# Performance work log

Hardware: AMD Instinct MI355X
Metric: run time of the kernel (lower is better)

Reference implementation:

```python
import jax, jax.numpy as jnp
import numpy as np
import math

NN_K = 32          # num_neighbor = ceil(k/dilation) = 32
MAP_SIZE = 32
GROUP = 4


def _fibonacci_sphere(samples):
    # matches fibonacci_sphere(samples, randomize=False): rnd = 1.0
    pts = [[0.0, 0.0, 0.0]]
    offset = 2.0 / samples
    increment = math.pi * (3.0 - math.sqrt(5.0))
    for i in range(samples - 1):
        y = i * offset - 1 + offset / 2.0
        r = math.sqrt(1.0 - y * y)
        phi = ((i + 1.0) % samples) * increment
        pts.append([math.cos(phi) * r, y, math.sin(phi) * r])
    return np.asarray(pts, dtype=np.float32)


def setup_inputs() -> dict:
    B, N, C_in, C_out = 8, 2048, 64, 128
    key = jax.random.key(0)
    ks = jax.random.split(key, 6)
    x = jax.random.normal(ks[0], (B, 3, N), dtype=jnp.float32)
    feature = jax.random.normal(ks[1], (B, C_in, N), dtype=jnp.float32)
    neigh_indexs = jax.random.randint(ks[2], (B, N, NN_K), 0, N, dtype=jnp.int32)
    B_rff = jax.random.normal(ks[3], (7, MAP_SIZE), dtype=jnp.float32)  # frozen RFF proj
    kernels = jnp.asarray(_fibonacci_sphere(NN_K).T)                    # [3, NN_K], frozen
    mlp_w = jax.random.normal(ks[4], (C_in, 2 * MAP_SIZE), dtype=jnp.float32) * 0.05
    mlp_b = jnp.zeros((C_in,), dtype=jnp.float32)
    conv_w = jax.random.normal(ks[5], (C_out, 2 * C_in * NN_K), dtype=jnp.float32) * 0.02
    conv_b = jnp.zeros((C_out,), dtype=jnp.float32)
    return {"x": x, "feature": feature, "neigh_indexs": neigh_indexs,
            "B_rff": B_rff, "kernels": kernels,
            "mlp_w": mlp_w, "mlp_b": mlp_b, "conv_w": conv_w, "conv_b": conv_b}


def _topkmax(perm):
    # two normalization passes over axis=1 (rows), squaring in between, then hard threshold
    perm = perm / (jnp.sum(perm, axis=1, keepdims=True) + 1e-6)
    perm = perm * perm
    perm = perm / (jnp.sum(perm, axis=1, keepdims=True) + 1e-6)
    return jnp.where(perm > 0.1, perm, 0.0)


def _paiconv(x, feature, neigh_indexs, B_rff, kernels, mlp_w, mlp_b, conv_w, conv_b):
    bsz, C, N = feature.shape           # B, num_feat, num_pts
    nn_k = neigh_indexs.shape[-1]
    xp = jnp.transpose(x, (0, 2, 1))    # [B, N, 3]

    # neighbor gather of coordinates -> [B*N, nn, 3]
    x_neighs = jax.vmap(lambda p, i: p[i])(xp, neigh_indexs).reshape(bsz * N, nn_k, 3)
    x_rep = jnp.broadcast_to(x_neighs[:, :1, :], x_neighs.shape)
    x_rel = x_neighs - x_rep
    x_dis = jnp.linalg.norm(x_rel, axis=-1, keepdims=True)

    # random Fourier features + 1x1 conv (mlp)
    pos = (2.0 * math.pi) * jnp.concatenate([x_rep, x_rel, x_dis], axis=-1)  # [BN, nn, 7]
    xf = pos @ B_rff                                                          # [BN, nn, 32]
    xf = jnp.concatenate([jnp.sin(xf), jnp.cos(xf)], axis=-1)                 # [BN, nn, 64]
    xf = jnp.einsum('oc,bnc->bon', mlp_w, xf) + mlp_b[None, :, None]          # [BN, C, nn]

    # neighbor gather of features -> [BN, C, nn], concat with positional feats
    fp = jnp.transpose(feature, (0, 2, 1))                                    # [B, N, C]
    f_nb = jax.vmap(lambda p, i: p[i])(fp, neigh_indexs).reshape(bsz * N, nn_k, C)
    feats = jnp.concatenate([jnp.transpose(f_nb, (0, 2, 1)), xf], axis=1)     # [BN, 2C, nn]

    # permutation/attention matrix
    one_pad = jnp.zeros((nn_k, nn_k), dtype=x.dtype).at[0, 0].set(1.0)
    perm = x_rel @ kernels + one_pad                                          # [BN, nn, nn]
    perm = jnp.where(perm > 0, perm, 0.0)
    perm = _topkmax(perm)

    if C > 3:  # static channel shuffle with group=4
        feats = feats.reshape(bsz * N, GROUP, 2 * C // GROUP, nn_k)
        feats = jnp.transpose(feats, (0, 2, 1, 3)).reshape(bsz * N, 2 * C, nn_k)

    feats = feats @ perm                                                      # [BN, 2C, nn]
    feats = feats.reshape(bsz * N, 2 * C * nn_k)
    out = feats @ conv_w.T + conv_b                                           # [BN, out_c]
    return jnp.transpose(out.reshape(bsz, N, -1), (0, 2, 1))                  # [B, out_c, N]


def reference(x, feature, neigh_indexs, B_rff, kernels, mlp_w, mlp_b, conv_w, conv_b):
    return _paiconv(x, feature, neigh_indexs, B_rff, kernels, mlp_w, mlp_b, conv_w, conv_b)
```

## Files before the change

### kernel.cpp

```cpp
#include <hip/hip_runtime.h>
#include <hip/hip_bf16.h>

typedef unsigned short ushort_t;
typedef __attribute__((ext_vector_type(8))) short short8;
typedef __attribute__((ext_vector_type(4))) float floatx4;

#define TWO_PI 6.28318530717958647692f

__device__ __forceinline__ float bf2f(ushort_t u) {
  union { unsigned u; float f; } v; v.u = ((unsigned)u) << 16; return v.f;
}
__device__ __forceinline__ unsigned pk(float a, float b) {
  union { __hip_bfloat162 h2; unsigned u; } v;
  v.h2 = __float22bfloat162_rn(make_float2(a, b));
  return v.u;
}
__device__ __forceinline__ float ldin(const void* p, int idx, bool bf) {
  return bf ? bf2f(((const ushort_t*)p)[idx]) : ((const float*)p)[idx];
}
__device__ __forceinline__ bool detect_bf16(const void* xv) {
  const ushort_t* us = (const ushort_t*)xv;
  unsigned u = us[threadIdx.x & 63];
  int e = (u >> 7) & 0xFF;
  bool good = (e >= 110) && (e <= 133);
  unsigned long long m = __ballot(good);
  return __builtin_popcountll(m) >= 52;
}
__device__ __forceinline__ uint4 pack8f(const float* p) {
  float4 a = *(const float4*)p, b = *(const float4*)(p + 4);
  uint4 r;
  r.x = pk(a.x, a.y); r.y = pk(a.z, a.w);
  r.z = pk(b.x, b.y); r.w = pk(b.z, b.w);
  return r;
}

__global__ __launch_bounds__(256) void paiconv_prep(
    const void* __restrict__ xprobe, const void* __restrict__ feat,
    ushort_t* __restrict__ Ft, const void* __restrict__ W,
    ushort_t* __restrict__ Wc)
{
  const bool bfm = detect_bf16(xprobe);
  const int t = threadIdx.x;
  __shared__ ushort_t tile[64 * 72];

  if (blockIdx.x >= 256) {
    int i = ((blockIdx.x - 256) * 256 + t) << 3;
    int n = i >> 12, rem = i & 4095;
    int c = rem >> 5, j = rem & 31;
    int src = (n << 12) + (((c & 31) * 4 + (c >> 5)) << 5) + j;
    if (bfm) *(uint4*)(Wc + i) = *(const uint4*)((const ushort_t*)W + src);
    else     *(uint4*)(Wc + i) = pack8f((const float*)W + src);
    return;
  }

  const int bb = blockIdx.x >> 5;
  const int n0 = (blockIdx.x & 31) << 6;
  {
    const int c = t & 63, ng = t >> 6;
    size_t base = (((size_t)(bb * 64 + c)) << 11) + n0 + (ng << 4);
    ushort_t v[16];
    if (bfm) {
      const ushort_t* fp_ = (const ushort_t*)feat + base;
      uint4 a = *(const uint4*)fp_, b2 = *(const uint4*)(fp_ + 8);
      unsigned uu[8] = {a.x, a.y, a.z, a.w, b2.x, b2.y, b2.z, b2.w};
#pragma unroll
      for (int e = 0; e < 8; ++e) {
        v[2 * e] = (ushort_t)(uu[e] & 0xffff);
        v[2 * e + 1] = (ushort_t)(uu[e] >> 16);
      }
    } else {
      const float* fp_ = (const float*)feat + base;
#pragma unroll
      for (int k = 0; k < 16; k += 2) {
        unsigned u = pk(fp_[k], fp_[k + 1]);
        v[k] = (ushort_t)(u & 0xffff);
        v[k + 1] = (ushort_t)(u >> 16);
      }
    }
#pragma unroll
    for (int k = 0; k < 16; ++k) tile[(ng * 16 + k) * 72 + c] = v[k];
  }
  __syncthreads();
  {
    const int nn = t >> 2, qtr = t & 3;
    uint4 w0 = *(const uint4*)(tile + nn * 72 + qtr * 16);
    uint4 w1 = *(const uint4*)(tile + nn * 72 + qtr * 16 + 8);
    ushort_t* dst = Ft + (((size_t)(bb * 2048 + n0 + nn)) << 6) + (qtr << 4);
    *(uint4*)dst = w0;
    *(uint4*)(dst + 8) = w1;
  }
}

#define SFPT 5184
__global__ __launch_bounds__(256) void paiconv_phase1(
    const void* __restrict__ x,
    const ushort_t* __restrict__ Ft,
    const int*  __restrict__ nbr,
    const void* __restrict__ Brff,
    const void* __restrict__ kern,
    const void* __restrict__ mlpw,
    const void* __restrict__ mlpb,
    ushort_t*   __restrict__ Ag)
{
  const bool bfm = detect_bf16(x);
  const int t = threadIdx.x;
  const int p0 = blockIdx.x << 1;
  const int b  = p0 >> 11;
  const int w = t >> 6, lane = t & 63, lrow = lane & 15, quad = lane >> 4;

  __shared__ ushort_t sRt[64 * 72];
  __shared__ ushort_t sF[SFPT];
  __shared__ ushort_t sP[2 * 32 * 40];
  __shared__ float sRel[2][32][3];
  __shared__ float sDis[2][32];
  __shared__ float sRep[2][3];
  __shared__ float sBr[224];

  const int gpt = t >> 7, gj = (t >> 2) & 31, gch = t & 3;
  const int gidx = nbr[((p0 + gpt) << 5) + gj];
  const ushort_t* gfr = Ft + (((size_t)(b * 2048 + gidx)) << 6) + (gch << 4);
  uint4 g0 = ((const uint4*)gfr)[0];
  uint4 g1 = ((const uint4*)gfr)[1];

  const int pj = t & 31;
  const float kn0 = ldin(kern, pj, bfm);
  const float kn1 = ldin(kern, 32 + pj, bfm);
  const float kn2 = ldin(kern, 64 + pj, bfm);
  const int mc = (w << 4) + lrow;
  const float bv = ldin(mlpb, mc, bfm);

  short8 mb0, mb1;
  if (bfm) {
    const ushort_t* mp = (const ushort_t*)mlpw + mc * 64;
    mb0 = *(const short8*)(mp + (quad << 3));
    mb1 = *(const short8*)(mp + 32 + (quad << 3));
  } else {
    const float* mp = (const float*)mlpw + mc * 64;
    uint4 u0 = pack8f(mp + (quad << 3));
    uint4 u1 = pack8f(mp + 32 + (quad << 3));
    mb0 = *(short8*)&u0;
    mb1 = *(short8*)&u1;
  }

  if (t < 224) sBr[t] = ldin(Brff, t, bfm);
  if (t < 64) {
    int pt = t >> 5, i = t & 31;
    int p = p0 + pt;
    int idx  = nbr[(p << 5) + i];
    int idx0 = nbr[(p << 5)];
    int xo = b * 6144;
    float rx = ldin(x, xo + idx0, bfm);
    float ry = ldin(x, xo + 2048 + idx0, bfm);
    float rz = ldin(x, xo + 4096 + idx0, bfm);
    float cx = ldin(x, xo + idx, bfm);
    float cy = ldin(x, xo + 2048 + idx, bfm);
    float cz = ldin(x, xo + 4096 + idx, bfm);
    float dx = cx - rx, dy = cy - ry, dz = cz - rz;
    sRel[pt][i][0] = dx; sRel[pt][i][1] = dy; sRel[pt][i][2] = dz;
    sDis[pt][i] = sqrtf(dx * dx + dy * dy + dz * dz);
    if (i == 0) { sRep[pt][0] = rx; sRep[pt][1] = ry; sRep[pt][2] = rz; }
  }
  __syncthreads();

  {
    int jn = t >> 2, mh = (t & 3) << 3;
    int pt = jn >> 5, j = jn & 31;
    float pos[7];
    pos[0] = TWO_PI * sRep[pt][0]; pos[1] = TWO_PI * sRep[pt][1];
    pos[2] = TWO_PI * sRep[pt][2];
    pos[3] = TWO_PI * sRel[pt][j][0]; pos[4] = TWO_PI * sRel[pt][j][1];
    pos[5] = TWO_PI * sRel[pt][j][2];
    pos[6] = TWO_PI * sDis[pt][j];
    unsigned sw[4], cw[4];
#pragma unroll
    for (int mm = 0; mm < 8; mm += 2) {
      float a0 = 0.f, a1 = 0.f;
#pragma unroll
      for (int d = 0; d < 7; ++d) {
        a0 += pos[d] * sBr[d * 32 + mh + mm];
        a1 += pos[d] * sBr[d * 32 + mh + mm + 1];
      }
      sw[mm >> 1] = pk(__sinf(a0), __sinf(a1));
      cw[mm >> 1] = pk(__cosf(a0), __cosf(a1));
    }
    ushort_t* rb = sRt + jn * 72;
    *(uint4*)(rb + mh)      = make_uint4(sw[0], sw[1], sw[2], sw[3]);
    *(uint4*)(rb + 32 + mh) = make_uint4(cw[0], cw[1], cw[2], cw[3]);
  }
  if (t < 128) {
    int pt = t >> 6, h = (t >> 5) & 1;
    float col[16];
    float s1 = 0.f;
#pragma unroll
    for (int il = 0; il < 16; ++il) {
      int i = h * 16 + il;
      float v = sRel[pt][i][0] * kn0 + sRel[pt][i][1] * kn1 + sRel[pt][i][2] * kn2;
      if (i == 0 && pj == 0) v += 1.0f;
      v = fmaxf(v, 0.f);
      col[il] = v; s1 += v;
    }
    s1 += __shfl_xor(s1, 32, 64);
    float inv1 = 1.0f / (s1 + 1e-6f);
    float s2 = 0.f;
#pragma unroll
    for (int il = 0; il < 16; ++il) { float v = col[il] * inv1; v = v * v; col[il] = v; s2 += v; }
    s2 += __shfl_xor(s2, 32, 64);
    float inv2 = 1.0f / (s2 + 1e-6f);
    unsigned pw[8];
#pragma unroll
    for (int il = 0; il < 16; il += 2) {
      float v0 = col[il] * inv2;     v0 = (v0 > 0.1f) ? v0 : 0.f;
      float v1 = col[il + 1] * inv2; v1 = (v1 > 0.1f) ? v1 : 0.f;
      pw[il >> 1] = pk(v0, v1);
    }
    ushort_t* dst = sP + pt * 1280 + pj * 40 + h * 16;
    *(uint4*)dst       = make_uint4(pw[0], pw[1], pw[2], pw[3]);
    *(uint4*)(dst + 8) = make_uint4(pw[4], pw[5], pw[6], pw[7]);
  }
  __syncthreads();

  const int rbase = (64 + mc) * 40 + ((4 + w) << 3);

#pragma unroll
  for (int pt = 0; pt < 2; ++pt) {
    {
#pragma unroll
      for (int half = 0; half < 2; ++half) {
        int mt = pt * 2 + half;
        const ushort_t* rp = sRt + (mt * 16 + lrow) * 72 + (quad << 3);
        short8 a0 = *(const short8*)rp;
        short8 a1 = *(const short8*)(rp + 32);
        floatx4 acc = {0.f, 0.f, 0.f, 0.f};
        acc = __builtin_amdgcn_mfma_f32_16x16x32_bf16(a0, mb0, acc, 0, 0, 0);
        acc = __builtin_amdgcn_mfma_f32_16x16x32_bf16(a1, mb1, acc, 0, 0, 0);
        int j0 = (half << 4) + (quad << 2);
        *(uint2*)(sF + rbase + j0) =
            make_uint2(pk(acc[0] + bv, acc[1] + bv), pk(acc[2] + bv, acc[3] + bv));
      }
      if (gpt == pt) {
        ushort_t* fp_ = sF + gch * 648 + gj;
        unsigned uu[8] = {g0.x, g0.y, g0.z, g0.w, g1.x, g1.y, g1.z, g1.w};
#pragma unroll
        for (int u = 0; u < 8; ++u) {
          fp_[(2 * u) * 40]     = (ushort_t)(uu[u] & 0xffff);
          fp_[(2 * u + 1) * 40] = (ushort_t)(uu[u] >> 16);
        }
      }
    }
    __syncthreads();

    {
      const ushort_t* Pp = sP + pt * 1280;
      short8 a0 = *(const short8*)(Pp + lrow * 40 + (quad << 3));
      short8 a1 = *(const short8*)(Pp + (16 + lrow) * 40 + (quad << 3));
      size_t prow = ((size_t)(p0 + pt)) << 12;
#pragma unroll
      for (int nt = 0; nt < 2; ++nt) {
        int blk = w * 2 + nt;
        int cidx = (blk << 4) + lrow;
        short8 bfg = *(const short8*)(sF + cidx * 40 + (blk << 3) + (quad << 3));
        floatx4 z = {0.f, 0.f, 0.f, 0.f};
        floatx4 c0 = __builtin_amdgcn_mfma_f32_16x16x32_bf16(a0, bfg, z, 0, 0, 0);
        floatx4 c1 = __builtin_amdgcn_mfma_f32_16x16x32_bf16(a1, bfg, z, 0, 0, 0);
        ushort_t* ad = Ag + prow + cidx * 32 + (quad << 2);
        *(uint2*)ad        = make_uint2(pk(c0[0], c0[1]), pk(c0[2], c0[3]));
        *(uint2*)(ad + 16) = make_uint2(pk(c1[0], c1[1]), pk(c1[2], c1[3]));
      }
    }
    if (pt == 0) __syncthreads();
  }
}

__global__ __launch_bounds__(512) void paiconv_gemm(
    const ushort_t* __restrict__ A,
    const ushort_t* __restrict__ Wc,
    float* __restrict__ part)
{
  __shared__ ushort_t lA[2][64 * 72];
  __shared__ ushort_t lB[2][128 * 72];
  const int m0 = blockIdx.x << 6;
  const int K0 = blockIdx.y << 11;
  const int t = threadIdx.x;
  const int w = t >> 6, lane = t & 63;
  const int wm = w & 1, wn = w >> 1, lrow = lane & 15, quad = lane >> 4;

  const int ar = t >> 3, ac = (t & 7) << 3;
  const int wr = t >> 2, wc = (t & 3) << 4;
  const ushort_t* Ap = A + (size_t)(m0 + ar) * 4096 + K0 + ac;
  const ushort_t* Wp = Wc + (size_t)wr * 4096 + K0 + wc;

  uint4 ea0 = *(const uint4*)Ap;
  uint4 eb0 = *(const uint4*)Wp,        eb1 = *(const uint4*)(Wp + 8);
  uint4 oa0 = *(const uint4*)(Ap + 64);
  uint4 ob0 = *(const uint4*)(Wp + 64), ob1 = *(const uint4*)(Wp + 72);

  floatx4 acc[2][2];
#pragma unroll
  for (int i = 0; i < 2; ++i)
#pragma unroll
    for (int j = 0; j < 2; ++j) acc[i][j] = (floatx4){0.f, 0.f, 0.f, 0.f};

  for (int kb = 0; kb < 32; kb += 2) {
    {
      ushort_t* la = lA[0];
      ushort_t* lb = lB[0];
      *(uint4*)(la + ar * 72 + ac)     = ea0;
      *(uint4*)(lb + wr * 72 + wc)     = eb0;
      *(uint4*)(lb + wr * 72 + wc + 8) = eb1;
      __syncthreads();
      if (kb + 2 < 32) {
        int off = (kb + 2) << 6;
        ea0 = *(const uint4*)(Ap + off);
        eb0 = *(const uint4*)(Wp + off); eb1 = *(const uint4*)(Wp + off + 8);
      }
#pragma unroll
      for (int kk = 0; kk < 2; ++kk) {
        short8 af0 = *(const short8*)(la + ((wm << 5) + lrow) * 72 + (kk << 5) + (quad << 3));
        short8 af1 = *(const short8*)(la + ((wm << 5) + 16 + lrow) * 72 + (kk << 5) + (quad << 3));
#pragma unroll
        for (int ni = 0; ni < 2; ++ni) {
          short8 bf = *(const short8*)(lb + ((wn << 5) + (ni << 4) + lrow) * 72 +
                                       (kk << 5) + (quad << 3));
          acc[0][ni] = __builtin_amdgcn_mfma_f32_16x16x32_bf16(af0, bf, acc[0][ni], 0, 0, 0);
          acc[1][ni] = __builtin_amdgcn_mfma_f32_16x16x32_bf16(af1, bf, acc[1][ni], 0, 0, 0);
        }
      }
    }
    {
      ushort_t* la = lA[1];
      ushort_t* lb = lB[1];
      *(uint4*)(la + ar * 72 + ac)     = oa0;
      *(uint4*)(lb + wr * 72 + wc)     = ob0;
      *(uint4*)(lb + wr * 72 + wc + 8) = ob1;
      __syncthreads();
      if (kb + 3 < 32) {
        int off = (kb + 3) << 6;
        oa0 = *(const uint4*)(Ap + off);
        ob0 = *(const uint4*)(Wp + off); ob1 = *(const uint4*)(Wp + off + 8);
      }
#pragma unroll
      for (int kk = 0; kk < 2; ++kk) {
        short8 af0 = *(const short8*)(la + ((wm << 5) + lrow) * 72 + (kk << 5) + (quad << 3));
        short8 af1 = *(const short8*)(la + ((wm << 5) + 16 + lrow) * 72 + (kk << 5) + (quad << 3));
#pragma unroll
        for (int ni = 0; ni < 2; ++ni) {
          short8 bf = *(const short8*)(lb + ((wn << 5) + (ni << 4) + lrow) * 72 +
                                       (kk << 5) + (quad << 3));
          acc[0][ni] = __builtin_amdgcn_mfma_f32_16x16x32_bf16(af0, bf, acc[0][ni], 0, 0, 0);
          acc[1][ni] = __builtin_amdgcn_mfma_f32_16x16x32_bf16(af1, bf, acc[1][ni], 0, 0, 0);
        }
      }
    }
  }

  float* dst = part + ((size_t)blockIdx.y << 21);
#pragma unroll
  for (int mi = 0; mi < 2; ++mi)
#pragma unroll
    for (int ni = 0; ni < 2; ++ni)
#pragma unroll
      for (int r = 0; r < 4; ++r) {
        int m = m0 + (wm << 5) + (mi << 4) + (quad << 2) + r;
        int n = (wn << 5) + (ni << 4) + lrow;
        dst[(size_t)m * 128 + n] = acc[mi][ni][r];
      }
}

__global__ __launch_bounds__(256) void paiconv_reduce(
    const void* __restrict__ xprobe, const float* __restrict__ part,
    const void* __restrict__ bias, void* __restrict__ out)
{
  const bool bfm = detect_bf16(xprobe);
  __shared__ float buf[128 * 65];
  const int m0 = blockIdx.x << 6;
  const int b = m0 >> 11, n0 = m0 & 2047;
  const int t = threadIdx.x;

#pragma unroll
  for (int i = 0; i < 8; ++i) {
    int idx = (i * 256 + t) << 2;
    int mt = idx >> 7, c = idx & 127;
    size_t o = (size_t)(m0 + mt) * 128 + c;
    float4 v0 = *(const float4*)(part + o);
    float4 v1 = *(const float4*)(part + (1u << 21) + o);
    buf[(c + 0) * 65 + mt] = v0.x + v1.x + ldin(bias, c + 0, bfm);
    buf[(c + 1) * 65 + mt] = v0.y + v1.y + ldin(bias, c + 1, bfm);
    buf[(c + 2) * 65 + mt] = v0.z + v1.z + ldin(bias, c + 2, bfm);
    buf[(c + 3) * 65 + mt] = v0.w + v1.w + ldin(bias, c + 3, bfm);
  }
  __syncthreads();
#pragma unroll
  for (int i = 0; i < 8; ++i) {
    int idx = (i * 256 + t) << 2;
    int c = idx >> 6, nl = idx & 63;
    float v0 = buf[c * 65 + nl], v1 = buf[c * 65 + nl + 1];
    float v2 = buf[c * 65 + nl + 2], v3 = buf[c * 65 + nl + 3];
    size_t o = (size_t)b * 262144 + (size_t)c * 2048 + n0 + nl;
    if (bfm) *(uint2*)((ushort_t*)out + o) = make_uint2(pk(v0, v1), pk(v2, v3));
    else     *(float4*)((float*)out + o) = make_float4(v0, v1, v2, v3);
  }
}

extern "C" void kernel_launch(void* const* d_in, const int* in_sizes, int n_in,
                              void* d_out, int out_size, void* d_ws, size_t ws_size,
                              hipStream_t stream) {
  const void* x     = d_in[0];
  const void* feat  = d_in[1];
  const int*  nbr   = (const int*)d_in[2];
  const void* Brff  = d_in[3];
  const void* kern  = d_in[4];
  const void* mlpw  = d_in[5];
  const void* mlpb  = d_in[6];
  const void* convw = d_in[7];
  const void* convb = d_in[8];

  char* ws = (char*)d_ws;
  ushort_t* A   = (ushort_t*)ws;
  ushort_t* Wcv = (ushort_t*)(ws + (size_t)134217728);
  float*    prt = (float*)(ws + (size_t)135266304);
  ushort_t* Ft  = (ushort_t*)(ws + (size_t)152043520);

  paiconv_prep<<<512, 256, 0, stream>>>(x, feat, Ft, convw, Wcv);
  paiconv_phase1<<<8192, 256, 0, stream>>>(x, Ft, nbr, Brff, kern, mlpw, mlpb, A);
  paiconv_gemm<<<dim3(256, 2, 1), 512, 0, stream>>>(A, Wcv, prt);
  paiconv_reduce<<<256, 256, 0, stream>>>(x, prt, convb, d_out);
}
```

Baseline: 164.6 us.

## Use direct global-to-LDS loads with XOR-swizzled layout in split-K GEMM

Replaces the register-staged global loads followed by LDS stores in the GEMM kernel with global_load_lds intrinsics that write straight into shared memory, double-buffered with one sync per k-step. Drops the padded 72-stride LDS layout in favour of a 64-stride layout with XOR chunk swizzling to avoid bank conflicts on the MFMA fragment reads. This removes VGPR staging and LDS write instructions. It relies on the implicit wave-contiguous LDS destination layout matching the swizzle, and on the sync ordering being enough for the asynchronous loads to complete.

```diff
diff --git a/kernel.cpp b/kernel.cpp
--- a/kernel.cpp
+++ b/kernel.cpp
@@ -32,6 +32,12 @@
   r.x = pk(a.x, a.y); r.y = pk(a.z, a.w);
   r.z = pk(b.x, b.y); r.w = pk(b.z, b.w);
   return r;
+}
+
+__device__ __forceinline__ void gload16(const void* g, void* l) {
+  __builtin_amdgcn_global_load_lds(
+      (const __attribute__((address_space(1))) unsigned*)g,
+      (__attribute__((address_space(3))) unsigned*)l, 16, 0, 0);
 }
 
 __global__ __launch_bounds__(256) void paiconv_prep(
@@ -276,23 +282,21 @@
     const ushort_t* __restrict__ Wc,
     float* __restrict__ part)
 {
-  __shared__ ushort_t lA[2][64 * 72];
-  __shared__ ushort_t lB[2][128 * 72];
+  __shared__ ushort_t lAs[2 * 64 * 64];
+  __shared__ ushort_t lBs[2 * 128 * 64];
   const int m0 = blockIdx.x << 6;
   const int K0 = blockIdx.y << 11;
   const int t = threadIdx.x;
   const int w = t >> 6, lane = t & 63;
   const int wm = w & 1, wn = w >> 1, lrow = lane & 15, quad = lane >> 4;
-
-  const int ar = t >> 3, ac = (t & 7) << 3;
-  const int wr = t >> 2, wc = (t & 3) << 4;
-  const ushort_t* Ap = A + (size_t)(m0 + ar) * 4096 + K0 + ac;
-  const ushort_t* Wp = Wc + (size_t)wr * 4096 + K0 + wc;
-
-  uint4 ea0 = *(const uint4*)Ap;
-  uint4 eb0 = *(const uint4*)Wp,        eb1 = *(const uint4*)(Wp + 8);
-  uint4 oa0 = *(const uint4*)(Ap + 64);
-  uint4 ob0 = *(const uint4*)(Wp + 64), ob1 = *(const uint4*)(Wp + 72);
+  const int sx = lrow & 7;
+
+  const int srow = t >> 3, schk = t & 7;
+  const int gchk = schk ^ (srow & 7);
+  const ushort_t* Agp  = A  + (size_t)(m0 + srow) * 4096 + K0 + (gchk << 3);
+  const ushort_t* Bgp0 = Wc + (size_t)srow * 4096        + K0 + (gchk << 3);
+  const ushort_t* Bgp1 = Wc + (size_t)(64 + srow) * 4096 + K0 + (gchk << 3);
+  const int wb = w << 9;
 
   floatx4 acc[2][2];
 #pragma unroll
@@ -300,58 +304,35 @@
 #pragma unroll
     for (int j = 0; j < 2; ++j) acc[i][j] = (floatx4){0.f, 0.f, 0.f, 0.f};
 
-  for (int kb = 0; kb < 32; kb += 2) {
-    {
-      ushort_t* la = lA[0];
-      ushort_t* lb = lB[0];
-      *(uint4*)(la + ar * 72 + ac)     = ea0;
-      *(uint4*)(lb + wr * 72 + wc)     = eb0;
-      *(uint4*)(lb + wr * 72 + wc + 8) = eb1;
-      __syncthreads();
-      if (kb + 2 < 32) {
-        int off = (kb + 2) << 6;
-        ea0 = *(const uint4*)(Ap + off);
-        eb0 = *(const uint4*)(Wp + off); eb1 = *(const uint4*)(Wp + off + 8);
-      }
-#pragma unroll
-      for (int kk = 0; kk < 2; ++kk) {
-        short8 af0 = *(const short8*)(la + ((wm << 5) + lrow) * 72 + (kk << 5) + (quad << 3));
-        short8 af1 = *(const short8*)(la + ((wm << 5) + 16 + lrow) * 72 + (kk << 5) + (quad << 3));
-#pragma unroll
-        for (int ni = 0; ni < 2; ++ni) {
-          short8 bf = *(const short8*)(lb + ((wn << 5) + (ni << 4) + lrow) * 72 +
-                                       (kk << 5) + (quad << 3));
-          acc[0][ni] = __builtin_amdgcn_mfma_f32_16x16x32_bf16(af0, bf, acc[0][ni], 0, 0, 0);
-          acc[1][ni] = __builtin_amdgcn_mfma_f32_16x16x32_bf16(af1, bf, acc[1][ni], 0, 0, 0);
-        }
-      }
-    }
-    {
-      ushort_t* la = lA[1];
-      ushort_t* lb = lB[1];
-      *(uint4*)(la + ar * 72 + ac)     = oa0;
-      *(uint4*)(lb + wr * 72 + wc)     = ob0;
-      *(uint4*)(lb + wr * 72 + wc + 8) = ob1;
-      __syncthreads();
-      if (kb + 3 < 32) {
-        int off = (kb + 3) << 6;
-        oa0 = *(const uint4*)(Ap + off);
-        ob0 = *(const uint4*)(Wp + off); ob1 = *(const uint4*)(Wp + off + 8);
-      }
-#pragma unroll
-      for (int kk = 0; kk < 2; ++kk) {
-        short8 af0 = *(const short8*)(la + ((wm << 5) + lrow) * 72 + (kk << 5) + (quad << 3));
-        short8 af1 = *(const short8*)(la + ((wm << 5) + 16 + lrow) * 72 + (kk << 5) + (quad << 3));
-#pragma unroll
-        for (int ni = 0; ni < 2; ++ni) {
-          short8 bf = *(const short8*)(lb + ((wn << 5) + (ni << 4) + lrow) * 72 +
-                                       (kk << 5) + (quad << 3));
-          acc[0][ni] = __builtin_amdgcn_mfma_f32_16x16x32_bf16(af0, bf, acc[0][ni], 0, 0, 0);
-          acc[1][ni] = __builtin_amdgcn_mfma_f32_16x16x32_bf16(af1, bf, acc[1][ni], 0, 0, 0);
-        }
-      }
-    }
-  }
+#define STAGE(buf, kbn) do { int off_ = (kbn) << 6;                         \
+    gload16(Agp  + off_, lAs + ((buf) << 12) + wb);                         \
+    gload16(Bgp0 + off_, lBs + ((buf) << 13) + wb);                         \
+    gload16(Bgp1 + off_, lBs + ((buf) << 13) + 4096 + wb); } while (0)
+
+  STAGE(0, 0);
+  __syncthreads();
+
+  int cur = 0;
+  for (int kb = 0; kb < 32; ++kb) {
+    if (kb + 1 < 32) STAGE(cur ^ 1, kb + 1);
+    const ushort_t* la = lAs + (cur << 12);
+    const ushort_t* lb = lBs + (cur << 13);
+#pragma unroll
+    for (int kk = 0; kk < 2; ++kk) {
+      int ch = ((((kk << 2) + quad) ^ sx) << 3);
+      short8 af0 = *(const short8*)(la + (((wm << 5) + lrow) << 6) + ch);
+      short8 af1 = *(const short8*)(la + (((wm << 5) + 16 + lrow) << 6) + ch);
+#pragma unroll
+      for (int ni = 0; ni < 2; ++ni) {
+        short8 bf = *(const short8*)(lb + (((wn << 5) + (ni << 4) + lrow) << 6) + ch);
+        acc[0][ni] = __builtin_amdgcn_mfma_f32_16x16x32_bf16(af0, bf, acc[0][ni], 0, 0, 0);
+        acc[1][ni] = __builtin_amdgcn_mfma_f32_16x16x32_bf16(af1, bf, acc[1][ni], 0, 0, 0);
+      }
+    }
+    __syncthreads();
+    cur ^= 1;
+  }
+#undef STAGE
 
   float* dst = part + ((size_t)blockIdx.y << 21);
 #pragma unroll
```

Result: no change. 162.4 us (-1.3%).
